# Kernel tuning notes

Hardware: AMD Instinct MI355X
Metric: run time of the kernel (lower is better)

Reference implementation:

```python
import jax, jax.numpy as jnp
import numpy as np

E = 1024
H = 16
DFF = 4 * E
EPS = 1e-5


def layer_norm(x, scale, bias):
    mu = jnp.mean(x, axis=-1, keepdims=True)
    var = jnp.var(x, axis=-1, keepdims=True)
    return (x - mu) * jax.lax.rsqrt(var + EPS) * scale + bias


def setup_inputs() -> dict:
    key = jax.random.key(0)
    ks = jax.random.split(key, 12)
    N, L = 2, 2048
    x = jax.random.normal(ks[0], (N, L, E), dtype=jnp.float32)
    attn_mask = jax.random.randint(ks[1], (N, H, L, L), 0, 2) == 1
    s = 0.02
    return {
        "x": x,
        "attn_mask": attn_mask,
        "ln1_s": jnp.ones((E,), jnp.float32),
        "ln1_b": jnp.zeros((E,), jnp.float32),
        "Wqkv": jax.random.normal(ks[2], (E, 3 * E), jnp.float32) * s,
        "bqkv": jnp.zeros((3 * E,), jnp.float32),
        "Wo": jax.random.normal(ks[3], (E, E), jnp.float32) * s,
        "bo": jnp.zeros((E,), jnp.float32),
        "ln2_s": jnp.ones((E,), jnp.float32),
        "ln2_b": jnp.zeros((E,), jnp.float32),
        "lnf_s": jnp.ones((E,), jnp.float32),
        "lnf_b": jnp.zeros((E,), jnp.float32),
        "W1": jax.random.normal(ks[4], (E, DFF), jnp.float32) * s,
        "b1": jnp.zeros((DFF,), jnp.float32),
        "W2": jax.random.normal(ks[5], (DFF, E), jnp.float32) * s,
        "b2": jnp.zeros((E,), jnp.float32),
    }


def reference(x, attn_mask, ln1_s, ln1_b, Wqkv, bqkv, Wo, bo,
              ln2_s, ln2_b, lnf_s, lnf_b, W1, b1, W2, b2):
    N, L, _ = x.shape
    D = E // H
    # --- self attention (pre-norm) ---
    h = layer_norm(x, ln1_s, ln1_b)
    qkv = h @ Wqkv + bqkv                      # [N,L,3E]
    q, k, v = jnp.split(qkv, 3, axis=-1)
    q = q.reshape(N, L, H, D)
    k = k.reshape(N, L, H, D)
    v = v.reshape(N, L, H, D)
    a = jnp.einsum('nqhd,nkhd->nhqk', q, k) * (D ** -0.5)  # [N,H,L,L]
    a = jnp.where(attn_mask, -jnp.inf, a)
    a = jax.nn.softmax(a, axis=-1)
    o = jnp.einsum('nhqk,nkhd->nqhd', a, v).reshape(N, L, E)
    o = o @ Wo + bo
    x = x + o
    # --- feedforward (norm_2 then FF's internal LN) ---
    h = layer_norm(x, ln2_s, ln2_b)
    h = layer_norm(h, lnf_s, lnf_b)
    h = jax.nn.gelu(h @ W1 + b1, approximate=False) @ W2 + b2
    return x + h
```

## Files before the change

### kernel.cpp

```cpp
#include <hip/hip_runtime.h>
#include <math.h>

#define E_DIM 1024
#define H_HEADS 16
#define D_HEAD 64
#define DFF_DIM 4096
#define L_SEQ 2048
#define N_BATCH 2
#define T_TOK (N_BATCH * L_SEQ)

typedef __attribute__((ext_vector_type(8))) __bf16 bf16x8;
typedef __attribute__((ext_vector_type(4))) float f32x4;

__device__ __forceinline__ unsigned short f2bf(float f) {
  union { float f; unsigned int u; } v; v.f = f;
  unsigned int r = v.u + 0x7fffu + ((v.u >> 16) & 1u);
  return (unsigned short)(r >> 16);
}

__device__ __forceinline__ void gld16(const void* g, void* l) {
  __builtin_amdgcn_global_load_lds(
      (const __attribute__((address_space(1))) unsigned int*)g,
      (__attribute__((address_space(3))) unsigned int*)l, 16, 0, 0);
}

__global__ __launch_bounds__(256) void convert_transpose(
    const float* __restrict__ in, unsigned short* __restrict__ out, int K, int N) {
  __shared__ float tile[32][33];
  int n0 = blockIdx.x * 32, k0 = blockIdx.y * 32;
  int tx = threadIdx.x & 31, ty = threadIdx.x >> 5;
#pragma unroll
  for (int i = 0; i < 32; i += 8)
    tile[ty + i][tx] = in[(size_t)(k0 + ty + i) * N + n0 + tx];
  __syncthreads();
#pragma unroll
  for (int i = 0; i < 32; i += 8)
    out[(size_t)(n0 + ty + i) * K + k0 + tx] = f2bf(tile[tx][ty + i]);
}

__device__ __forceinline__ void block_reduce2(float& a, float& b, float* sm, int tid) {
#pragma unroll
  for (int off = 32; off > 0; off >>= 1) {
    a += __shfl_down(a, off);
    b += __shfl_down(b, off);
  }
  int wid = tid >> 6;
  if ((tid & 63) == 0) { sm[wid * 2] = a; sm[wid * 2 + 1] = b; }
  __syncthreads();
  a = sm[0] + sm[2] + sm[4] + sm[6];
  b = sm[1] + sm[3] + sm[5] + sm[7];
}

__global__ __launch_bounds__(256) void ln_kernel(
    const float* __restrict__ x, const float* __restrict__ s,
    const float* __restrict__ b, unsigned short* __restrict__ out) {
  int row = blockIdx.x, tid = threadIdx.x;
  __shared__ float sm[8];
  float4 v = ((const float4*)(x + (size_t)row * E_DIM))[tid];
  float sum = v.x + v.y + v.z + v.w;
  float sq = v.x * v.x + v.y * v.y + v.z * v.z + v.w * v.w;
  block_reduce2(sum, sq, sm, tid);
  float mu = sum * (1.0f / E_DIM);
  float var = sq * (1.0f / E_DIM) - mu * mu;
  float rs = rsqrtf(var + 1e-5f);
  float4 sv = ((const float4*)s)[tid];
  float4 bv = ((const float4*)b)[tid];
  ushort4 o4;
  o4.x = f2bf((v.x - mu) * rs * sv.x + bv.x);
  o4.y = f2bf((v.y - mu) * rs * sv.y + bv.y);
  o4.z = f2bf((v.z - mu) * rs * sv.z + bv.z);
  o4.w = f2bf((v.w - mu) * rs * sv.w + bv.w);
  ((ushort4*)(out + (size_t)row * E_DIM))[tid] = o4;
}

__global__ __launch_bounds__(256) void ln2_kernel(
    const float* __restrict__ x, const float* __restrict__ s2,
    const float* __restrict__ b2, const float* __restrict__ sf,
    const float* __restrict__ bf_, unsigned short* __restrict__ out) {
  int row = blockIdx.x, tid = threadIdx.x;
  __shared__ float sm[8];
  float4 v = ((const float4*)(x + (size_t)row * E_DIM))[tid];
  float sum = v.x + v.y + v.z + v.w;
  float sq = v.x * v.x + v.y * v.y + v.z * v.z + v.w * v.w;
  block_reduce2(sum, sq, sm, tid);
  float mu = sum * (1.0f / E_DIM);
  float rs = rsqrtf(sq * (1.0f / E_DIM) - mu * mu + 1e-5f);
  float4 s2v = ((const float4*)s2)[tid];
  float4 b2v = ((const float4*)b2)[tid];
  float y0 = (v.x - mu) * rs * s2v.x + b2v.x;
  float y1 = (v.y - mu) * rs * s2v.y + b2v.y;
  float y2 = (v.z - mu) * rs * s2v.z + b2v.z;
  float y3 = (v.w - mu) * rs * s2v.w + b2v.w;
  float sum2 = y0 + y1 + y2 + y3;
  float sq2 = y0 * y0 + y1 * y1 + y2 * y2 + y3 * y3;
  __syncthreads();
  block_reduce2(sum2, sq2, sm, tid);
  float mu2 = sum2 * (1.0f / E_DIM);
  float rs2 = rsqrtf(sq2 * (1.0f / E_DIM) - mu2 * mu2 + 1e-5f);
  float4 sfv = ((const float4*)sf)[tid];
  float4 bfv = ((const float4*)bf_)[tid];
  ushort4 o4;
  o4.x = f2bf((y0 - mu2) * rs2 * sfv.x + bfv.x);
  o4.y = f2bf((y1 - mu2) * rs2 * sfv.y + bfv.y);
  o4.z = f2bf((y2 - mu2) * rs2 * sfv.z + bfv.z);
  o4.w = f2bf((y3 - mu2) * rs2 * sfv.w + bfv.w);
  ((ushort4*)(out + (size_t)row * E_DIM))[tid] = o4;
}

template <int EPI>
__global__ __launch_bounds__(256) void gemm_bt(
    const unsigned short* __restrict__ A, const unsigned short* __restrict__ Bt,
    const float* __restrict__ bias, const float* __restrict__ resid,
    void* __restrict__ outp, int M, int N, int K) {
  __shared__ unsigned short As[128 * 32];
  __shared__ unsigned short Bs[128 * 32];
  int tid = threadIdx.x;
  int lane = tid & 63, wave = tid >> 6;
  int m0 = blockIdx.y * 128, n0 = blockIdx.x * 128;
  int wm = (wave & 1) * 64, wn = (wave >> 1) * 64;
  int lm = lane & 15, lq = lane >> 4;
  int srow = wave * 32 + (lane >> 2);
  int scol = (lane & 3) * 8;
  const unsigned short* Ag = A + (size_t)(m0 + srow) * K + scol;
  const unsigned short* Bg = Bt + (size_t)(n0 + srow) * K + scol;
  unsigned short* AsW = As + wave * 1024;
  unsigned short* BsW = Bs + wave * 1024;
  f32x4 acc[4][4] = {};
  for (int k0 = 0; k0 < K; k0 += 32) {
    __syncthreads();
    gld16(Ag + k0, AsW);
    gld16(Ag + (size_t)16 * K + k0, AsW + 512);
    gld16(Bg + k0, BsW);
    gld16(Bg + (size_t)16 * K + k0, BsW + 512);
    __syncthreads();
    bf16x8 a[4], b[4];
#pragma unroll
    for (int i = 0; i < 4; i++)
      a[i] = *(const bf16x8*)(As + (wm + i * 16 + lm) * 32 + lq * 8);
#pragma unroll
    for (int j = 0; j < 4; j++)
      b[j] = *(const bf16x8*)(Bs + (wn + j * 16 + lm) * 32 + lq * 8);
#pragma unroll
    for (int i = 0; i < 4; i++)
#pragma unroll
      for (int j = 0; j < 4; j++)
        acc[i][j] = __builtin_amdgcn_mfma_f32_16x16x32_bf16(a[i], b[j], acc[i][j], 0, 0, 0);
  }
#pragma unroll
  for (int i = 0; i < 4; i++)
#pragma unroll
    for (int j = 0; j < 4; j++) {
      int row = m0 + wm + i * 16 + lq * 4;
      int col = n0 + wn + j * 16 + lm;
      float bcol = bias[col];
#pragma unroll
      for (int r = 0; r < 4; r++) {
        float v = acc[i][j][r] + bcol;
        size_t idx = (size_t)(row + r) * N + col;
        if (EPI == 0) {
          ((unsigned short*)outp)[idx] = f2bf(v);
        } else if (EPI == 1) {
          float g = 0.5f * v * (1.0f + erff(v * 0.70710678118f));
          ((unsigned short*)outp)[idx] = f2bf(g);
        } else {
          ((float*)outp)[idx] = resid[idx] + v;
        }
      }
    }
}

__global__ __launch_bounds__(256) void attn_kernel(
    const unsigned short* __restrict__ qkv, const int* __restrict__ mask,
    unsigned short* __restrict__ o) {
  const int bq = blockIdx.x;
  const int nh = blockIdx.y;
  const int h = nh & 15;
  const int tid = threadIdx.x, lane = tid & 63, wave = tid >> 6;
  const int lm = lane & 15, lq = lane >> 4;

  __shared__ unsigned short Ks[64 * 72];
  __shared__ unsigned short Vt[64 * 72];
  __shared__ unsigned short Ps[4][16 * 72];

  const int q_base = bq * 64;
  const int tok0 = (nh >> 4) * L_SEQ;
  const int qoff = h * 64, koff = E_DIM + h * 64, voff = 2 * E_DIM + h * 64;
  const int* mbase = mask + (size_t)nh * L_SEQ * L_SEQ;

  bf16x8 qf[2];
  {
    int t = tok0 + q_base + wave * 16 + lm;
    const unsigned short* qr = qkv + (size_t)t * (3 * E_DIM) + qoff + lq * 8;
    qf[0] = *(const bf16x8*)(qr);
    qf[1] = *(const bf16x8*)(qr + 32);
  }

  float m_run[4], l_run[4];
  f32x4 oacc[4] = {};
#pragma unroll
  for (int r = 0; r < 4; r++) { m_run[r] = -1e30f; l_run[r] = 0.0f; }

  for (int kt = 0; kt < L_SEQ / 64; kt++) {
    const int k_base = kt * 64;
    __syncthreads();
    {
      int row = tid >> 3, chunk = tid & 7;
#pragma unroll
      for (int it = 0; it < 2; it++) {
        int key = row + it * 32;
        int t = tok0 + k_base + key;
        uint4 kv = *(const uint4*)(qkv + (size_t)t * (3 * E_DIM) + koff + chunk * 8);
        *(uint4*)(Ks + key * 72 + chunk * 8) = kv;
        uint4 vv = *(const uint4*)(qkv + (size_t)t * (3 * E_DIM) + voff + chunk * 8);
        const unsigned short* vs = (const unsigned short*)&vv;
        int kcol = key ^ (chunk << 3);
#pragma unroll
        for (int jj = 0; jj < 8; jj++)
          Vt[(chunk * 8 + jj) * 72 + kcol] = vs[jj];
      }
    }
    __syncthreads();

    f32x4 s[4];
#pragma unroll
    for (int nt = 0; nt < 4; nt++) {
      bf16x8 kb0 = *(const bf16x8*)(Ks + (nt * 16 + lm) * 72 + lq * 8);
      bf16x8 kb1 = *(const bf16x8*)(Ks + (nt * 16 + lm) * 72 + 32 + lq * 8);
      f32x4 acc = {};
      acc = __builtin_amdgcn_mfma_f32_16x16x32_bf16(qf[0], kb0, acc, 0, 0, 0);
      acc = __builtin_amdgcn_mfma_f32_16x16x32_bf16(qf[1], kb1, acc, 0, 0, 0);
      s[nt] = acc;
    }
    const int qrow = q_base + wave * 16 + lq * 4;
#pragma unroll
    for (int nt = 0; nt < 4; nt++) {
      int kcol = k_base + nt * 16 + lm;
#pragma unroll
      for (int r = 0; r < 4; r++) {
        float v = s[nt][r] * 0.125f;
        int mval = mbase[(size_t)(qrow + r) * L_SEQ + kcol];
        s[nt][r] = mval ? -1e30f : v;
      }
    }
    float alpha[4], rsum[4];
#pragma unroll
    for (int r = 0; r < 4; r++) {
      float v = fmaxf(fmaxf(s[0][r], s[1][r]), fmaxf(s[2][r], s[3][r]));
#pragma unroll
      for (int mo = 1; mo < 16; mo <<= 1) v = fmaxf(v, __shfl_xor(v, mo));
      float mn = fmaxf(m_run[r], v);
      alpha[r] = __expf(m_run[r] - mn);
      m_run[r] = mn;
      rsum[r] = 0.0f;
    }
    unsigned short* pw = Ps[wave];
#pragma unroll
    for (int nt = 0; nt < 4; nt++)
#pragma unroll
      for (int r = 0; r < 4; r++) {
        float p = __expf(s[nt][r] - m_run[r]);
        rsum[r] += p;
        pw[(lq * 4 + r) * 72 + nt * 16 + lm] = f2bf(p);
      }
#pragma unroll
    for (int r = 0; r < 4; r++) {
      float v = rsum[r];
#pragma unroll
      for (int mo = 1; mo < 16; mo <<= 1) v += __shfl_xor(v, mo);
      l_run[r] = l_run[r] * alpha[r] + v;
    }
#pragma unroll
    for (int j = 0; j < 4; j++)
#pragma unroll
      for (int r = 0; r < 4; r++) oacc[j][r] *= alpha[r];
    __syncthreads();

#pragma unroll
    for (int c = 0; c < 2; c++) {
      bf16x8 pa = *(const bf16x8*)(pw + lm * 72 + c * 32 + lq * 8);
#pragma unroll
      for (int j = 0; j < 4; j++) {
        int d = j * 16 + lm;
        int kblk = (c * 4 + lq) ^ ((d >> 3) & 7);
        bf16x8 vb = *(const bf16x8*)(Vt + d * 72 + kblk * 8);
        oacc[j] = __builtin_amdgcn_mfma_f32_16x16x32_bf16(pa, vb, oacc[j], 0, 0, 0);
      }
    }
  }
  const int qrow = q_base + wave * 16 + lq * 4;
#pragma unroll
  for (int r = 0; r < 4; r++) {
    float inv_l = 1.0f / l_run[r];
    int t = tok0 + qrow + r;
#pragma unroll
    for (int j = 0; j < 4; j++)
      o[(size_t)t * E_DIM + h * 64 + j * 16 + lm] = f2bf(oacc[j][r] * inv_l);
  }
}

extern "C" void kernel_launch(void* const* d_in, const int* in_sizes, int n_in,
                              void* d_out, int out_size, void* d_ws, size_t ws_size,
                              hipStream_t stream) {
  const float* x = (const float*)d_in[0];
  const int* mask = (const int*)d_in[1];
  const float* ln1_s = (const float*)d_in[2];
  const float* ln1_b = (const float*)d_in[3];
  const float* Wqkv = (const float*)d_in[4];
  const float* bqkv = (const float*)d_in[5];
  const float* Wo = (const float*)d_in[6];
  const float* bo = (const float*)d_in[7];
  const float* ln2_s = (const float*)d_in[8];
  const float* ln2_b = (const float*)d_in[9];
  const float* lnf_s = (const float*)d_in[10];
  const float* lnf_b = (const float*)d_in[11];
  const float* W1 = (const float*)d_in[12];
  const float* b1 = (const float*)d_in[13];
  const float* W2 = (const float*)d_in[14];
  const float* b2 = (const float*)d_in[15];

  size_t off = 0;
  auto alloc = [&](size_t bytes) {
    void* p = (char*)d_ws + off;
    off += (bytes + 255) & ~(size_t)255;
    return p;
  };
  unsigned short* WqkvT = (unsigned short*)alloc((size_t)3072 * 1024 * 2);
  unsigned short* WoT = (unsigned short*)alloc((size_t)1024 * 1024 * 2);
  unsigned short* W1T = (unsigned short*)alloc((size_t)4096 * 1024 * 2);
  unsigned short* W2T = (unsigned short*)alloc((size_t)1024 * 4096 * 2);
  unsigned short* h1 = (unsigned short*)alloc((size_t)T_TOK * E_DIM * 2);
  unsigned short* qkvb = (unsigned short*)alloc((size_t)T_TOK * 3 * E_DIM * 2);
  unsigned short* ob = (unsigned short*)alloc((size_t)T_TOK * E_DIM * 2);
  float* x2 = (float*)alloc((size_t)T_TOK * E_DIM * 4);
  unsigned short* h2 = (unsigned short*)alloc((size_t)T_TOK * E_DIM * 2);
  unsigned short* g1 = (unsigned short*)alloc((size_t)T_TOK * DFF_DIM * 2);

  convert_transpose<<<dim3(3072 / 32, 1024 / 32), 256, 0, stream>>>(Wqkv, WqkvT, 1024, 3072);
  convert_transpose<<<dim3(1024 / 32, 1024 / 32), 256, 0, stream>>>(Wo, WoT, 1024, 1024);
  convert_transpose<<<dim3(4096 / 32, 1024 / 32), 256, 0, stream>>>(W1, W1T, 1024, 4096);
  convert_transpose<<<dim3(1024 / 32, 4096 / 32), 256, 0, stream>>>(W2, W2T, 4096, 1024);
  ln_kernel<<<T_TOK, 256, 0, stream>>>(x, ln1_s, ln1_b, h1);
  gemm_bt<0><<<dim3(3072 / 128, T_TOK / 128), 256, 0, stream>>>(
      h1, WqkvT, bqkv, nullptr, qkvb, T_TOK, 3072, 1024);
  attn_kernel<<<dim3(L_SEQ / 64, N_BATCH * H_HEADS), 256, 0, stream>>>(qkvb, mask, ob);
  gemm_bt<2><<<dim3(1024 / 128, T_TOK / 128), 256, 0, stream>>>(
      ob, WoT, bo, x, x2, T_TOK, 1024, 1024);
  ln2_kernel<<<T_TOK, 256, 0, stream>>>(x2, ln2_s, ln2_b, lnf_s, lnf_b, h2);
  gemm_bt<1><<<dim3(DFF_DIM / 128, T_TOK / 128), 256, 0, stream>>>(
      h2, W1T, b1, nullptr, g1, T_TOK, DFF_DIM, 1024);
  gemm_bt<2><<<dim3(1024 / 128, T_TOK / 128), 256, 0, stream>>>(
      g1, W2T, b2, x2, (float*)d_out, T_TOK, 1024, 4096);

  (void)in_sizes; (void)n_in; (void)out_size; (void)ws_size;
}
```

Before: 1.081 ms.

## Split-K the Wo and W2 GEMMs and fuse partial-sum reduction into LN/add kernels

The two N=1024 GEMMs (Wo and W2) only launched 256 blocks, which underfills the GPU. They are now split along K into 2 and 4 slices that write fp32 partial buffers. The partials are summed, together with bias and residual, inside the LN2 kernel (which now also writes x2) and in a new add4 kernel. This raises parallelism at the cost of extra fp32 partial traffic (tens of MB) and one added kernel launch.

```diff
diff --git a/kernel.cpp b/kernel.cpp
--- a/kernel.cpp
+++ b/kernel.cpp
@@ -73,13 +73,24 @@
   ((ushort4*)(out + (size_t)row * E_DIM))[tid] = o4;
 }
 
-__global__ __launch_bounds__(256) void ln2_kernel(
-    const float* __restrict__ x, const float* __restrict__ s2,
-    const float* __restrict__ b2, const float* __restrict__ sf,
-    const float* __restrict__ bf_, unsigned short* __restrict__ out) {
+__global__ __launch_bounds__(256) void ln2_fused_kernel(
+    const float* __restrict__ p0, const float* __restrict__ p1,
+    const float* __restrict__ x, const float* __restrict__ bo,
+    const float* __restrict__ s2, const float* __restrict__ b2,
+    const float* __restrict__ sf, const float* __restrict__ bf_,
+    float* __restrict__ x2, unsigned short* __restrict__ out) {
   int row = blockIdx.x, tid = threadIdx.x;
   __shared__ float sm[8];
-  float4 v = ((const float4*)(x + (size_t)row * E_DIM))[tid];
+  float4 a0 = ((const float4*)(p0 + (size_t)row * E_DIM))[tid];
+  float4 a1 = ((const float4*)(p1 + (size_t)row * E_DIM))[tid];
+  float4 xv = ((const float4*)(x + (size_t)row * E_DIM))[tid];
+  float4 bov = ((const float4*)bo)[tid];
+  float4 v;
+  v.x = a0.x + a1.x + xv.x + bov.x;
+  v.y = a0.y + a1.y + xv.y + bov.y;
+  v.z = a0.z + a1.z + xv.z + bov.z;
+  v.w = a0.w + a1.w + xv.w + bov.w;
+  ((float4*)(x2 + (size_t)row * E_DIM))[tid] = v;
   float sum = v.x + v.y + v.z + v.w;
   float sq = v.x * v.x + v.y * v.y + v.z * v.z + v.w * v.w;
   block_reduce2(sum, sq, sm, tid);
@@ -107,16 +118,38 @@
   ((ushort4*)(out + (size_t)row * E_DIM))[tid] = o4;
 }
 
+__global__ __launch_bounds__(256) void add4_kernel(
+    const float* __restrict__ p0, const float* __restrict__ p1,
+    const float* __restrict__ p2, const float* __restrict__ p3,
+    const float* __restrict__ resid, const float* __restrict__ bias,
+    float* __restrict__ out) {
+  int row = blockIdx.x, tid = threadIdx.x;
+  size_t base = (size_t)row * E_DIM;
+  float4 a0 = ((const float4*)(p0 + base))[tid];
+  float4 a1 = ((const float4*)(p1 + base))[tid];
+  float4 a2 = ((const float4*)(p2 + base))[tid];
+  float4 a3 = ((const float4*)(p3 + base))[tid];
+  float4 rv = ((const float4*)(resid + base))[tid];
+  float4 bv = ((const float4*)bias)[tid];
+  float4 o;
+  o.x = a0.x + a1.x + a2.x + a3.x + rv.x + bv.x;
+  o.y = a0.y + a1.y + a2.y + a3.y + rv.y + bv.y;
+  o.z = a0.z + a1.z + a2.z + a3.z + rv.z + bv.z;
+  o.w = a0.w + a1.w + a2.w + a3.w + rv.w + bv.w;
+  ((float4*)(out + base))[tid] = o;
+}
+
 template <int EPI>
 __global__ __launch_bounds__(256) void gemm_bt(
     const unsigned short* __restrict__ A, const unsigned short* __restrict__ Bt,
-    const float* __restrict__ bias, const float* __restrict__ resid,
-    void* __restrict__ outp, int M, int N, int K) {
+    const float* __restrict__ bias, void* __restrict__ outp,
+    int M, int N, int K, int Ks) {
   __shared__ unsigned short As[128 * 32];
   __shared__ unsigned short Bs[128 * 32];
   int tid = threadIdx.x;
   int lane = tid & 63, wave = tid >> 6;
   int m0 = blockIdx.y * 128, n0 = blockIdx.x * 128;
+  int kz = blockIdx.z * Ks;
   int wm = (wave & 1) * 64, wn = (wave >> 1) * 64;
   int lm = lane & 15, lq = lane >> 4;
   int srow = wave * 32 + (lane >> 2);
@@ -126,7 +159,7 @@
   unsigned short* AsW = As + wave * 1024;
   unsigned short* BsW = Bs + wave * 1024;
   f32x4 acc[4][4] = {};
-  for (int k0 = 0; k0 < K; k0 += 32) {
+  for (int k0 = kz; k0 < kz + Ks; k0 += 32) {
     __syncthreads();
     gld16(Ag + k0, AsW);
     gld16(Ag + (size_t)16 * K + k0, AsW + 512);
@@ -146,13 +179,14 @@
       for (int j = 0; j < 4; j++)
         acc[i][j] = __builtin_amdgcn_mfma_f32_16x16x32_bf16(a[i], b[j], acc[i][j], 0, 0, 0);
   }
+  float* pout = (EPI == 3) ? ((float*)outp + (size_t)blockIdx.z * M * N) : nullptr;
 #pragma unroll
   for (int i = 0; i < 4; i++)
 #pragma unroll
     for (int j = 0; j < 4; j++) {
       int row = m0 + wm + i * 16 + lq * 4;
       int col = n0 + wn + j * 16 + lm;
-      float bcol = bias[col];
+      float bcol = (EPI == 3) ? 0.0f : bias[col];
 #pragma unroll
       for (int r = 0; r < 4; r++) {
         float v = acc[i][j][r] + bcol;
@@ -163,7 +197,7 @@
           float g = 0.5f * v * (1.0f + erff(v * 0.70710678118f));
           ((unsigned short*)outp)[idx] = f2bf(g);
         } else {
-          ((float*)outp)[idx] = resid[idx] + v;
+          pout[idx] = v;
         }
       }
     }
@@ -334,22 +368,28 @@
   float* x2 = (float*)alloc((size_t)T_TOK * E_DIM * 4);
   unsigned short* h2 = (unsigned short*)alloc((size_t)T_TOK * E_DIM * 2);
   unsigned short* g1 = (unsigned short*)alloc((size_t)T_TOK * DFF_DIM * 2);
+  float* part = (float*)alloc((size_t)4 * T_TOK * E_DIM * 4);
+  const size_t PSTRIDE = (size_t)T_TOK * E_DIM;
 
   convert_transpose<<<dim3(3072 / 32, 1024 / 32), 256, 0, stream>>>(Wqkv, WqkvT, 1024, 3072);
   convert_transpose<<<dim3(1024 / 32, 1024 / 32), 256, 0, stream>>>(Wo, WoT, 1024, 1024);
   convert_transpose<<<dim3(4096 / 32, 1024 / 32), 256, 0, stream>>>(W1, W1T, 1024, 4096);
   convert_transpose<<<dim3(1024 / 32, 4096 / 32), 256, 0, stream>>>(W2, W2T, 4096, 1024);
   ln_kernel<<<T_TOK, 256, 0, stream>>>(x, ln1_s, ln1_b, h1);
-  gemm_bt<0><<<dim3(3072 / 128, T_TOK / 128), 256, 0, stream>>>(
-      h1, WqkvT, bqkv, nullptr, qkvb, T_TOK, 3072, 1024);
+  gemm_bt<0><<<dim3(3072 / 128, T_TOK / 128, 1), 256, 0, stream>>>(
+      h1, WqkvT, bqkv, qkvb, T_TOK, 3072, 1024, 1024);
   attn_kernel<<<dim3(L_SEQ / 64, N_BATCH * H_HEADS), 256, 0, stream>>>(qkvb, mask, ob);
-  gemm_bt<2><<<dim3(1024 / 128, T_TOK / 128), 256, 0, stream>>>(
-      ob, WoT, bo, x, x2, T_TOK, 1024, 1024);
-  ln2_kernel<<<T_TOK, 256, 0, stream>>>(x2, ln2_s, ln2_b, lnf_s, lnf_b, h2);
-  gemm_bt<1><<<dim3(DFF_DIM / 128, T_TOK / 128), 256, 0, stream>>>(
-      h2, W1T, b1, nullptr, g1, T_TOK, DFF_DIM, 1024);
-  gemm_bt<2><<<dim3(1024 / 128, T_TOK / 128), 256, 0, stream>>>(
-      g1, W2T, b2, x2, (float*)d_out, T_TOK, 1024, 4096);
+  gemm_bt<3><<<dim3(1024 / 128, T_TOK / 128, 2), 256, 0, stream>>>(
+      ob, WoT, nullptr, part, T_TOK, 1024, 1024, 512);
+  ln2_fused_kernel<<<T_TOK, 256, 0, stream>>>(
+      part, part + PSTRIDE, x, bo, ln2_s, ln2_b, lnf_s, lnf_b, x2, h2);
+  gemm_bt<1><<<dim3(DFF_DIM / 128, T_TOK / 128, 1), 256, 0, stream>>>(
+      h2, W1T, b1, g1, T_TOK, DFF_DIM, 1024, 1024);
+  gemm_bt<3><<<dim3(1024 / 128, T_TOK / 128, 4), 256, 0, stream>>>(
+      g1, W2T, nullptr, part, T_TOK, 1024, 4096, 1024);
+  add4_kernel<<<T_TOK, 256, 0, stream>>>(
+      part, part + PSTRIDE, part + 2 * PSTRIDE, part + 3 * PSTRIDE,
+      x2, b2, (float*)d_out);
 
   (void)in_sizes; (void)n_in; (void)out_size; (void)ws_size;
 }
```

Result: faster. 1.056 ms (-2.3%).
